# Optimization experiments

Hardware: AMD Instinct MI355X
Metric: run time of the kernel (lower is better)

Reference implementation:

```python
import jax, jax.numpy as jnp
import numpy as np

B, D, S, O = 32768, 1024, 64, 4  # batch, feature_dim, n_subjects, n_outputs


def setup_inputs() -> dict:
    key = jax.random.key(0)
    kx, ks, kw, kb = jax.random.split(key, 4)
    x = jax.random.normal(kx, (B, D), dtype=jnp.float32)          # backbone features
    subject_ids = jax.random.randint(ks, (B,), 0, S)              # per-sample head id
    W = jax.random.normal(kw, (S, D, O), dtype=jnp.float32) / np.float32(np.sqrt(D))
    b = jax.random.normal(kb, (S, O), dtype=jnp.float32) * 0.01
    return {"x": x, "subject_ids": subject_ids, "W": W, "b": b}


def reference(x, subject_ids, W, b):
    # Vectorized form of the per-subject loop:
    #   for sid in unique(subject_ids): outputs[idxs] = heads[sid](features[idxs])
    # Each head is Linear(D, O): out[i] = x[i] @ W[sid[i]] + b[sid[i]].
    Wg = jnp.take(W, subject_ids, axis=0)   # [B, D, O] gathered per-sample weights
    bg = jnp.take(b, subject_ids, axis=0)   # [B, O]
    return jnp.einsum('bd,bdo->bo', x, Wg) + bg
```

## Files before the change

kernel.cpp:

```cpp
#include <hip/hip_runtime.h>

constexpr int B = 32768;
constexpr int D = 1024;
constexpr int S = 64;
constexpr int O = 4;


constexpr int CHUNKS      = 32;
constexpr int CHUNK       = B / CHUNKS;
constexpr int SEG         = CHUNK / 4;
constexpr int MAIN_BLOCKS = S * CHUNKS;

typedef float f4 __attribute__((ext_vector_type(4)));

__global__ __launch_bounds__(256) void main_kernel(
    const float* __restrict__ x,
    const int*   __restrict__ sid,
    const float* __restrict__ W,
    const float* __restrict__ bias,
    float*       __restrict__ out)
{
    __shared__ float Wt[O * D];
    __shared__ int   list[4][SEG];

    const int t    = threadIdx.x;
    const int lane = t & 63;
    const int wave = t >> 6;
    const int s    = blockIdx.x >> 5;
    const int c    = blockIdx.x & 31;
    const int q    = lane >> 4;

    {
        const float4* Wp = (const float4*)(W + (size_t)s * (D * O));
        #pragma unroll
        for (int r = 0; r < 4; ++r) {
            const int d = r * 256 + t;
            const float4 w4 = Wp[d];
            Wt[0 * D + d] = w4.x;
            Wt[1 * D + d] = w4.y;
            Wt[2 * D + d] = w4.z;
            Wt[3 * D + d] = w4.w;
        }
    }

    const int seg = c * CHUNK + wave * SEG;
    int cnt = 0;
    #pragma unroll
    for (int r = 0; r < 4; ++r) {
        const int i = seg + r * 64 + lane;
        const bool m = (sid[i] == s);
        const unsigned long long mask = __ballot(m);
        const int rank = __popcll(mask & ((1ull << lane) - 1ull));
        if (m) list[wave][cnt + rank] = i;
        cnt += __popcll(mask);
    }

    __syncthreads();
    if (cnt == 0) return;

    const float bb  = bias[(s << 2) + q];
    const f4*   Wt4 = (const f4*)Wt;

    int rowC = __builtin_amdgcn_readfirstlane(list[wave][0]);
    f4 xb[4];
    {
        const f4* xr = (const f4*)(x + ((size_t)rowC << 10));
        #pragma unroll
        for (int j = 0; j < 4; ++j)
            xb[j] = __builtin_nontemporal_load(xr + 64 * j + lane);
    }

    #pragma unroll 1
    for (int k = 0; k < cnt; ++k) {
        const bool more = (k + 1 < cnt);
        const int rowN = more
            ? __builtin_amdgcn_readfirstlane(list[wave][k + 1]) : rowC;

        float a0 = 0.f, a1 = 0.f, a2 = 0.f, a3 = 0.f;
        #pragma unroll
        for (int j = 0; j < 4; ++j) {
            const f4 xv = xb[j];
            const f4 w0 = Wt4[0 * 256 + 64 * j + lane];
            const f4 w1 = Wt4[1 * 256 + 64 * j + lane];
            const f4 w2 = Wt4[2 * 256 + 64 * j + lane];
            const f4 w3 = Wt4[3 * 256 + 64 * j + lane];
            a0 += xv.x * w0.x; a1 += xv.x * w1.x;
            a2 += xv.x * w2.x; a3 += xv.x * w3.x;
            a0 += xv.y * w0.y; a1 += xv.y * w1.y;
            a2 += xv.y * w2.y; a3 += xv.y * w3.y;
            a0 += xv.z * w0.z; a1 += xv.z * w1.z;
            a2 += xv.z * w2.z; a3 += xv.z * w3.z;
            a0 += xv.w * w0.w; a1 += xv.w * w1.w;
            a2 += xv.w * w2.w; a3 += xv.w * w3.w;
        }

        if (more) {
            const f4* xr = (const f4*)(x + ((size_t)rowN << 10));
            #pragma unroll
            for (int j = 0; j < 4; ++j)
                xb[j] = __builtin_nontemporal_load(xr + 64 * j + lane);
        }

        #pragma unroll
        for (int m = 16; m <= 32; m <<= 1) {
            a0 += __shfl_xor(a0, m, 64);
            a1 += __shfl_xor(a1, m, 64);
            a2 += __shfl_xor(a2, m, 64);
            a3 += __shfl_xor(a3, m, 64);
        }
        float v = (q == 0) ? a0 : (q == 1) ? a1 : (q == 2) ? a2 : a3;
        #pragma unroll
        for (int m = 1; m <= 8; m <<= 1)
            v += __shfl_xor(v, m, 64);

        if ((lane & 15) == 0)
            out[((size_t)rowC << 2) + q] = v + bb;

        rowC = rowN;
    }
}

extern "C" void kernel_launch(void* const* d_in, const int* in_sizes, int n_in,
                              void* d_out, int out_size, void* d_ws, size_t ws_size,
                              hipStream_t stream) {
    const float* x    = (const float*)d_in[0];
    const int*   sid  = (const int*)d_in[1];
    const float* W    = (const float*)d_in[2];
    const float* bias = (const float*)d_in[3];
    float* out = (float*)d_out;

    main_kernel<<<MAIN_BLOCKS, 256, 0, stream>>>(x, sid, W, bias, out);
}
```

Baseline: 190.2 us.

## Stream x rows into LDS double buffer via async global_load_lds

Replaces register prefetch of the next x row with direct global-to-LDS async loads into a per-wave two-slot ring, issuing rows two iterations ahead and using explicit vmcnt waits. Also shrinks the row index list to 16-bit, hoists the bias load before the barrier, and uses nontemporal output stores. The aim is deeper memory latency hiding for the bandwidth-bound gather of x, at the cost of 32KB more LDS per block, which may lower occupancy, and fragile hand-counted waitcnt values.

```diff
diff --git a/kernel.cpp b/kernel.cpp
--- a/kernel.cpp
+++ b/kernel.cpp
@@ -20,8 +20,9 @@
     const float* __restrict__ bias,
     float*       __restrict__ out)
 {
-    __shared__ float Wt[O * D];
-    __shared__ int   list[4][SEG];
+    __shared__ float          Wt[O * D];
+    __shared__ unsigned short list[4][SEG];
+    __shared__ float          xring[4][2][D];
 
     const int t    = threadIdx.x;
     const int lane = t & 63;
@@ -31,11 +32,11 @@
     const int q    = lane >> 4;
 
     {
-        const float4* Wp = (const float4*)(W + (size_t)s * (D * O));
+        const f4* Wp = (const f4*)(W + (size_t)s * (D * O));
         #pragma unroll
         for (int r = 0; r < 4; ++r) {
             const int d = r * 256 + t;
-            const float4 w4 = Wp[d];
+            const f4 w4 = Wp[d];
             Wt[0 * D + d] = w4.x;
             Wt[1 * D + d] = w4.y;
             Wt[2 * D + d] = w4.z;
@@ -51,35 +52,59 @@
         const bool m = (sid[i] == s);
         const unsigned long long mask = __ballot(m);
         const int rank = __popcll(mask & ((1ull << lane) - 1ull));
-        if (m) list[wave][cnt + rank] = i;
+        if (m) list[wave][cnt + rank] = (unsigned short)i;
         cnt += __popcll(mask);
     }
+
+    const float bb = bias[(s << 2) + q];
 
     __syncthreads();
     if (cnt == 0) return;
 
-    const float bb  = bias[(s << 2) + q];
-    const f4*   Wt4 = (const f4*)Wt;
+    const f4* Wt4 = (const f4*)Wt;
 
-    int rowC = __builtin_amdgcn_readfirstlane(list[wave][0]);
-    f4 xb[4];
-    {
-        const f4* xr = (const f4*)(x + ((size_t)rowC << 10));
-        #pragma unroll
-        for (int j = 0; j < 4; ++j)
-            xb[j] = __builtin_nontemporal_load(xr + 64 * j + lane);
+#define ISSUE_ROW(ROW, SLOT) do {                                              \
+        const float* _g = x + ((size_t)(ROW) << 10) + 4 * lane;                \
+        _Pragma("unroll")                                                      \
+        for (int _j = 0; _j < 4; ++_j)                                         \
+            __builtin_amdgcn_global_load_lds(                                  \
+                (const __attribute__((address_space(1))) unsigned int*)        \
+                    (_g + _j * 256),                                           \
+                (__attribute__((address_space(3))) unsigned int*)              \
+                    (&xring[wave][(SLOT)][_j * 256]),                          \
+                16, 0, 2);                                                     \
+    } while (0)
+
+#define VMWAIT(N) do {                                                         \
+        asm volatile("s_waitcnt vmcnt(" #N ")" ::: "memory");                  \
+        __builtin_amdgcn_sched_barrier(0);                                     \
+    } while (0)
+
+    int rowCur = __builtin_amdgcn_readfirstlane((int)list[wave][0]);
+    ISSUE_ROW(rowCur, 0);
+    int rowNext = rowCur;
+    if (cnt > 1) {
+        rowNext = __builtin_amdgcn_readfirstlane((int)list[wave][1]);
+        ISSUE_ROW(rowNext, 1);
     }
 
     #pragma unroll 1
     for (int k = 0; k < cnt; ++k) {
-        const bool more = (k + 1 < cnt);
-        const int rowN = more
-            ? __builtin_amdgcn_readfirstlane(list[wave][k + 1]) : rowC;
+        if (k == 0) {
+            if (cnt > 1) VMWAIT(4);
+            else         VMWAIT(0);
+        } else if (k < cnt - 1) {
+            VMWAIT(5);
+        } else {
+            VMWAIT(1);
+        }
+
+        const f4* xs = (const f4*)&xring[wave][k & 1][0];
 
         float a0 = 0.f, a1 = 0.f, a2 = 0.f, a3 = 0.f;
         #pragma unroll
         for (int j = 0; j < 4; ++j) {
-            const f4 xv = xb[j];
+            const f4 xv = xs[64 * j + lane];
             const f4 w0 = Wt4[0 * 256 + 64 * j + lane];
             const f4 w1 = Wt4[1 * 256 + 64 * j + lane];
             const f4 w2 = Wt4[2 * 256 + 64 * j + lane];
@@ -92,13 +117,6 @@
             a2 += xv.z * w2.z; a3 += xv.z * w3.z;
             a0 += xv.w * w0.w; a1 += xv.w * w1.w;
             a2 += xv.w * w2.w; a3 += xv.w * w3.w;
-        }
-
-        if (more) {
-            const f4* xr = (const f4*)(x + ((size_t)rowN << 10));
-            #pragma unroll
-            for (int j = 0; j < 4; ++j)
-                xb[j] = __builtin_nontemporal_load(xr + 64 * j + lane);
         }
 
         #pragma unroll
@@ -114,10 +132,22 @@
             v += __shfl_xor(v, m, 64);
 
         if ((lane & 15) == 0)
-            out[((size_t)rowC << 2) + q] = v + bb;
+            __builtin_nontemporal_store(v + bb,
+                                        &out[((size_t)rowCur << 2) + q]);
 
-        rowC = rowN;
+        if (k + 2 < cnt) {
+            const int rowP =
+                __builtin_amdgcn_readfirstlane((int)list[wave][k + 2]);
+            ISSUE_ROW(rowP, k & 1);
+            rowCur = rowNext;
+            rowNext = rowP;
+        } else {
+            rowCur = rowNext;
+        }
     }
+
+#undef ISSUE_ROW
+#undef VMWAIT
 }
 
 extern "C" void kernel_launch(void* const* d_in, const int* in_sizes, int n_in,
```

Measured after the change: 200.7 us. 5.5% more time.

## Balance matched rows across waves within block and double chunk count

Applied to the files above, without the earlier changes.

Doubles the number of batch chunks per subject so there are twice as many blocks, each scanning half as many sample ids. Each wave's matched rows are stored in shared memory as 16-bit indices, and the per-wave counts are combined into a single block-wide list. Waves then take rows round-robin from that list instead of each processing only its own segment. This aims to fix load imbalance when one wave's segment has more matches than the others, and to give more parallelism. The cost is extra scan work overall, a reload of the weight slice per block, and branching index lookups.

```diff
diff --git a/kernel.cpp b/kernel.cpp
--- a/kernel.cpp
+++ b/kernel.cpp
@@ -6,9 +6,9 @@
 constexpr int O = 4;
 
 
-constexpr int CHUNKS      = 32;
+constexpr int CHUNKS      = 64;
 constexpr int CHUNK       = B / CHUNKS;
-constexpr int SEG         = CHUNK / 4;
+constexpr int WSEG        = CHUNK / 4;
 constexpr int MAIN_BLOCKS = S * CHUNKS;
 
 typedef float f4 __attribute__((ext_vector_type(4)));
@@ -20,22 +20,23 @@
     const float* __restrict__ bias,
     float*       __restrict__ out)
 {
-    __shared__ float Wt[O * D];
-    __shared__ int   list[4][SEG];
+    __shared__ float          Wt[O * D];
+    __shared__ unsigned short wlist[4][WSEG];
+    __shared__ int            wcnt[4];
 
     const int t    = threadIdx.x;
     const int lane = t & 63;
     const int wave = t >> 6;
-    const int s    = blockIdx.x >> 5;
-    const int c    = blockIdx.x & 31;
+    const int s    = blockIdx.x >> 6;
+    const int c    = blockIdx.x & 63;
     const int q    = lane >> 4;
 
     {
-        const float4* Wp = (const float4*)(W + (size_t)s * (D * O));
+        const f4* Wp = (const f4*)(W + (size_t)s * (D * O));
         #pragma unroll
         for (int r = 0; r < 4; ++r) {
             const int d = r * 256 + t;
-            const float4 w4 = Wp[d];
+            const f4 w4 = Wp[d];
             Wt[0 * D + d] = w4.x;
             Wt[1 * D + d] = w4.y;
             Wt[2 * D + d] = w4.z;
@@ -43,25 +44,41 @@
         }
     }
 
-    const int seg = c * CHUNK + wave * SEG;
+    const int seg = c * CHUNK + wave * WSEG;
     int cnt = 0;
     #pragma unroll
-    for (int r = 0; r < 4; ++r) {
+    for (int r = 0; r < 2; ++r) {
         const int i = seg + r * 64 + lane;
         const bool m = (sid[i] == s);
         const unsigned long long mask = __ballot(m);
         const int rank = __popcll(mask & ((1ull << lane) - 1ull));
-        if (m) list[wave][cnt + rank] = i;
+        if (m) wlist[wave][cnt + rank] = (unsigned short)i;
         cnt += __popcll(mask);
     }
+    if (lane == 0) wcnt[wave] = cnt;
+
+    const float bb = bias[(s << 2) + q];
 
     __syncthreads();
-    if (cnt == 0) return;
 
-    const float bb  = bias[(s << 2) + q];
-    const f4*   Wt4 = (const f4*)Wt;
+    const int c0 = wcnt[0], c1 = wcnt[1], c2 = wcnt[2], c3 = wcnt[3];
+    const int p1 = c0, p2 = c0 + c1, p3 = c0 + c1 + c2;
+    const int total = p3 + c3;
 
-    int rowC = __builtin_amdgcn_readfirstlane(list[wave][0]);
+#define ROW_OF(G, DST) do {                                                    \
+        int _g = (G), _r;                                                      \
+        if      (_g < p1) _r = wlist[0][_g];                                   \
+        else if (_g < p2) _r = wlist[1][_g - p1];                              \
+        else if (_g < p3) _r = wlist[2][_g - p2];                              \
+        else              _r = wlist[3][_g - p3];                              \
+        (DST) = __builtin_amdgcn_readfirstlane(_r);                            \
+    } while (0)
+
+    int g = wave;
+    if (g >= total) return;
+
+    int rowC;
+    ROW_OF(g, rowC);
     f4 xb[4];
     {
         const f4* xr = (const f4*)(x + ((size_t)rowC << 10));
@@ -70,11 +87,13 @@
             xb[j] = __builtin_nontemporal_load(xr + 64 * j + lane);
     }
 
+    const f4* Wt4 = (const f4*)Wt;
+
     #pragma unroll 1
-    for (int k = 0; k < cnt; ++k) {
-        const bool more = (k + 1 < cnt);
-        const int rowN = more
-            ? __builtin_amdgcn_readfirstlane(list[wave][k + 1]) : rowC;
+    for (; g < total; g += 4) {
+        const bool more = (g + 4 < total);
+        int rowN = rowC;
+        if (more) ROW_OF(g + 4, rowN);
 
         float a0 = 0.f, a1 = 0.f, a2 = 0.f, a3 = 0.f;
         #pragma unroll
@@ -118,6 +137,8 @@
 
         rowC = rowN;
     }
+
+#undef ROW_OF
 }
 
 extern "C" void kernel_launch(void* const* d_in, const int* in_sizes, int n_in,
```

Result: no change. 187.1 us (-1.6%).
